# Performance work log

Measured on AMD Instinct MI355X. Metric: run time of the kernel, lower is better.

Reference implementation:

```python
import jax, jax.numpy as jnp
import numpy as np

N = 16384       # num nodes
E = 65536       # num edges (before self loops)
IN_DIM = 1536
HID = 1024
HEADS = 8
HD = HID // HEADS  # 128
NEG_SLOPE = 0.2
EPS = 1e-5


def _xavier(key, shape):
    fan_in, fan_out = shape[0], shape[-1]
    s = jnp.sqrt(6.0 / (fan_in + fan_out)).astype(jnp.float32)
    return jax.random.uniform(key, shape, jnp.float32, -s, s)


def setup_inputs() -> dict:
    key = jax.random.key(0)
    ks = jax.random.split(key, 32)
    inp = {
        "x": jax.random.normal(ks[0], (N, IN_DIM), jnp.float32),
        "edge_index": jax.random.randint(ks[1], (2, E), 0, N, dtype=jnp.int32),
        # input projection + norm1
        "W_in": _xavier(ks[2], (IN_DIM, HID)), "b_in": jnp.zeros((HID,), jnp.float32),
        "ln1_g": jnp.ones((HID,), jnp.float32), "ln1_b": jnp.zeros((HID,), jnp.float32),
        # GATv2 layer 1
        "g1_Wl": _xavier(ks[3], (HID, HID)), "g1_bl": jnp.zeros((HID,), jnp.float32),
        "g1_Wr": _xavier(ks[4], (HID, HID)), "g1_br": jnp.zeros((HID,), jnp.float32),
        "g1_att": _xavier(ks[5], (HEADS, HD)), "g1_bo": jnp.zeros((HID,), jnp.float32),
        "ln2_g": jnp.ones((HID,), jnp.float32), "ln2_b": jnp.zeros((HID,), jnp.float32),
        # GATv2 layer 2
        "g2_Wl": _xavier(ks[6], (HID, HID)), "g2_bl": jnp.zeros((HID,), jnp.float32),
        "g2_Wr": _xavier(ks[7], (HID, HID)), "g2_br": jnp.zeros((HID,), jnp.float32),
        "g2_att": _xavier(ks[8], (HEADS, HD)), "g2_bo": jnp.zeros((HID,), jnp.float32),
        "ln3_g": jnp.ones((HID,), jnp.float32), "ln3_b": jnp.zeros((HID,), jnp.float32),
        # scorer MLP 1024 -> 512 -> 128 -> 1
        "Ws1": _xavier(ks[9], (HID, 512)), "bs1": jnp.zeros((512,), jnp.float32),
        "Ws2": _xavier(ks[10], (512, 128)), "bs2": jnp.zeros((128,), jnp.float32),
        "Ws3": _xavier(ks[11], (128, 1)), "bs3": jnp.zeros((1,), jnp.float32),
    }
    return inp


def layer_norm(x, g, b):
    mu = jnp.mean(x, axis=-1, keepdims=True)
    var = jnp.var(x, axis=-1, keepdims=True)
    return (x - mu) * jax.lax.rsqrt(var + EPS) * g + b


def gatv2(h, src, dst, Wl, bl, Wr, br, att, bo):
    # GATv2Conv: x_j = lin_l(h)[src], x_i = lin_r(h)[dst]
    xl = (h @ Wl + bl).reshape(N, HEADS, HD)
    xr = (h @ Wr + br).reshape(N, HEADS, HD)
    e = jax.nn.leaky_relu(xl[src] + xr[dst], NEG_SLOPE)      # [E', H, C]
    logit = jnp.einsum('ehc,hc->eh', e, att)                  # [E', H]
    m = jax.ops.segment_max(logit, dst, num_segments=N)       # segment softmax over dst
    a = jnp.exp(logit - m[dst])
    denom = jax.ops.segment_sum(a, dst, num_segments=N)
    alpha = a / denom[dst]
    out = jax.ops.segment_sum(alpha[:, :, None] * xl[src], dst, num_segments=N)
    return out.reshape(N, HID) + bo


def reference(x, edge_index, W_in, b_in, ln1_g, ln1_b,
              g1_Wl, g1_bl, g1_Wr, g1_br, g1_att, g1_bo, ln2_g, ln2_b,
              g2_Wl, g2_bl, g2_Wr, g2_br, g2_att, g2_bo, ln3_g, ln3_b,
              Ws1, bs1, Ws2, bs2, Ws3, bs3):
    # PyG GATv2Conv adds self-loops by default
    loop = jnp.arange(N, dtype=edge_index.dtype)
    src = jnp.concatenate([edge_index[0], loop])
    dst = jnp.concatenate([edge_index[1], loop])

    h = jax.nn.gelu(layer_norm(x @ W_in + b_in, ln1_g, ln1_b), approximate=False)
    h1 = gatv2(h, src, dst, g1_Wl, g1_bl, g1_Wr, g1_br, g1_att, g1_bo)
    h = h + jax.nn.gelu(layer_norm(h1, ln2_g, ln2_b), approximate=False)
    h2 = gatv2(h, src, dst, g2_Wl, g2_bl, g2_Wr, g2_br, g2_att, g2_bo)
    h = h + jax.nn.gelu(layer_norm(h2, ln3_g, ln3_b), approximate=False)

    s = jax.nn.silu(h @ Ws1 + bs1)
    s = jax.nn.silu(s @ Ws2 + bs2)
    scores = (s @ Ws3 + bs3).squeeze(-1)   # [N]
    return scores, h
```

## Files before the change

kernel.cpp:

```cpp
#include <hip/hip_runtime.h>
#include <hip/hip_bf16.h>
#include <math.h>

#define N_NODES 16384
#define E_EDGES 65536
#define ET (E_EDGES + N_NODES)
#define IN_DIM 1536
#define HID 1024
#define XSTR 2048

typedef __attribute__((ext_vector_type(8))) short bf16x8;
typedef __attribute__((ext_vector_type(4))) float f32x4;

__device__ __forceinline__ unsigned short f2b(float f) {
  unsigned int u = __float_as_uint(f);
  u = (u + 0x7FFFu + ((u >> 16) & 1u)) >> 16;
  return (unsigned short)u;
}

__device__ __forceinline__ float b2f(unsigned short u) {
  return __uint_as_float((unsigned int)u << 16);
}

__device__ __forceinline__ void gload_lds16(const void* g, void* l) {
  __builtin_amdgcn_global_load_lds((const __attribute__((address_space(1))) void*)g,
                                   (__attribute__((address_space(3))) void*)l, 16, 0, 0);
}

__device__ __forceinline__ float gelu_exact(float y) {
  return 0.5f * y * (1.0f + erff(y * 0.70710678118654752f));
}

__global__ void conv_bf16_kernel(const float* __restrict__ in, unsigned short* __restrict__ out, int n4) {
  int i = blockIdx.x * 256 + threadIdx.x;
  if (i < n4) {
    float4 v = ((const float4*)in)[i];
    ushort4 o;
    o.x = f2b(v.x); o.y = f2b(v.y); o.z = f2b(v.z); o.w = f2b(v.w);
    ((ushort4*)out)[i] = o;
  }
}

__global__ void transpose_conv_kernel(const float* __restrict__ in, unsigned short* __restrict__ out,
                                      int K, int N) {
  __shared__ float tile[32][33];
  int bx = blockIdx.x * 32;
  int by = blockIdx.y * 32;
  int tx = threadIdx.x, ty = threadIdx.y;
  #pragma unroll
  for (int i = 0; i < 32; i += 8)
    tile[ty + i][tx] = in[(size_t)(by + ty + i) * N + bx + tx];
  __syncthreads();
  #pragma unroll
  for (int i = 0; i < 32; i += 8)
    out[(size_t)(bx + ty + i) * K + by + tx] = f2b(tile[tx][ty + i]);
}

__global__ void concat2_kernel(const float* __restrict__ a, const float* __restrict__ b,
                               float* __restrict__ o, int n) {
  int i = blockIdx.x * 256 + threadIdx.x;
  if (i < n) o[i] = a[i];
  else if (i < 2 * n) o[i] = b[i - n];
}

template <int ACT, int WB>
__global__ __launch_bounds__(512)
void gemm_bf16_kernel(const unsigned short* __restrict__ A, const unsigned short* __restrict__ Bt,
                      const float* __restrict__ bias, float* __restrict__ C,
                      unsigned short* __restrict__ Cb, int M, int N, int K, int nx) {
  __shared__ unsigned short As[256 * 64];
  __shared__ unsigned short Bs[128 * 64];
  const int t = threadIdx.x;
  const int l = t & 63;
  const int w = t >> 6;
  const int wr = w >> 1, wc = w & 1;

  const int nwg = gridDim.x;
  const int bid = blockIdx.x;
  int tile = bid;
  if ((nwg & 7) == 0) {
    const int cpx = nwg >> 3;
    tile = (bid & 7) * cpx + (bid >> 3);
  }
  const int bm = (tile / nx) * 256;
  const int bn = (tile % nx) * 128;

  f32x4 acc[4][4];
  #pragma unroll
  for (int m = 0; m < 4; m++)
    #pragma unroll
    for (int n = 0; n < 4; n++) acc[m][n] = (f32x4){0.f, 0.f, 0.f, 0.f};

  const int srow = t >> 3;
  const int scolbsw = ((t & 7) * 16) ^ ((srow & 7) << 4);
  const unsigned short* Ag = A + (size_t)(bm + srow) * K + (scolbsw >> 1);
  const unsigned short* Bg = Bt + (size_t)(bn + srow) * K + (scolbsw >> 1);

  const int ar = wr * 64 + (l & 15);
  const int br = wc * 64 + (l & 15);
  const int kk2 = (l >> 4) * 16;
  const int swA = (ar & 7) << 4;
  const int swB = (br & 7) << 4;
  const char* Asb = (const char*)As;
  const char* Bsb = (const char*)Bs;

  for (int k0 = 0; k0 < K; k0 += 64) {
    #pragma unroll
    for (int i = 0; i < 4; i++)
      gload_lds16(Ag + (size_t)i * 64 * K + k0, (char*)As + t * 16 + i * 8192);
    #pragma unroll
    for (int i = 0; i < 2; i++)
      gload_lds16(Bg + (size_t)i * 64 * K + k0, (char*)Bs + t * 16 + i * 8192);
    __syncthreads();
    bf16x8 af[4], bfr[4];
    #pragma unroll
    for (int kh = 0; kh < 2; kh++) {
      const int kb = kk2 + kh * 64;
      #pragma unroll
      for (int m = 0; m < 4; m++)
        af[m] = *(const bf16x8*)(Asb + (ar + m * 16) * 128 + (kb ^ swA));
      #pragma unroll
      for (int n = 0; n < 4; n++)
        bfr[n] = *(const bf16x8*)(Bsb + (br + n * 16) * 128 + (kb ^ swB));
      #pragma unroll
      for (int m = 0; m < 4; m++)
        #pragma unroll
        for (int n = 0; n < 4; n++)
          acc[m][n] = __builtin_amdgcn_mfma_f32_16x16x32_bf16(af[m], bfr[n], acc[m][n], 0, 0, 0);
    }
    __syncthreads();
  }

  const int crow0 = bm + wr * 64 + (l >> 4) * 4;
  const int ccol0 = bn + wc * 64 + (l & 15);
  #pragma unroll
  for (int m = 0; m < 4; m++) {
    #pragma unroll
    for (int n = 0; n < 4; n++) {
      int col = ccol0 + n * 16;
      float bv = bias[col];
      #pragma unroll
      for (int v = 0; v < 4; v++) {
        int row = crow0 + m * 16 + v;
        float x = acc[m][n][v] + bv;
        if (ACT == 1) x = x / (1.0f + expf(-x));
        if (WB != 2) C[(size_t)row * N + col] = x;
        if (WB != 0) Cb[(size_t)row * N + col] = f2b(x);
      }
    }
  }
}

__global__ __launch_bounds__(256)
void ln_gelu_kernel(const float* __restrict__ c, const float* __restrict__ g,
                    const float* __restrict__ b, float* __restrict__ h,
                    unsigned short* __restrict__ hb) {
  int row = blockIdx.x;
  int t = threadIdx.x;
  const float* cr = c + (size_t)row * HID;
  float v[4];
  float s = 0.f, q = 0.f;
  #pragma unroll
  for (int j = 0; j < 4; j++) {
    v[j] = cr[t + 256 * j];
    s += v[j];
    q += v[j] * v[j];
  }
  #pragma unroll
  for (int off = 32; off; off >>= 1) {
    s += __shfl_xor(s, off);
    q += __shfl_xor(q, off);
  }
  __shared__ float rs[4], rq[4];
  int wv = t >> 6, l = t & 63;
  if (l == 0) { rs[wv] = s; rq[wv] = q; }
  __syncthreads();
  s = rs[0] + rs[1] + rs[2] + rs[3];
  q = rq[0] + rq[1] + rq[2] + rq[3];
  float mu = s * (1.0f / HID);
  float var = q * (1.0f / HID) - mu * mu;
  float rstd = rsqrtf(var + 1e-5f);
  float* hr = h + (size_t)row * HID;
  unsigned short* hbr = hb + (size_t)row * HID;
  #pragma unroll
  for (int j = 0; j < 4; j++) {
    int ci = t + 256 * j;
    float y = (v[j] - mu) * rstd * g[ci] + b[ci];
    float z = gelu_exact(y);
    hr[ci] = z;
    hbr[ci] = f2b(z);
  }
}

__global__ void build_edges_kernel(const int* __restrict__ ei, int* __restrict__ srcA,
                                   int* __restrict__ dstA, int* __restrict__ deg) {
  int i = blockIdx.x * 256 + threadIdx.x;
  if (i >= ET) return;
  int s, d;
  if (i < E_EDGES) { s = ei[i]; d = ei[E_EDGES + i]; }
  else             { s = i - E_EDGES; d = s; }
  srcA[i] = s;
  dstA[i] = d;
  atomicAdd(&deg[d], 1);
}

__global__ __launch_bounds__(1024)
void scan16k_kernel(const int* __restrict__ deg, int* __restrict__ rowstart) {
  __shared__ int s[1024];
  int t = threadIdx.x;
  int local[16];
  int sum = 0;
  #pragma unroll
  for (int i = 0; i < 16; i++) { local[i] = deg[t * 16 + i]; sum += local[i]; }
  s[t] = sum;
  __syncthreads();
  for (int off = 1; off < 1024; off <<= 1) {
    int v = (t >= off) ? s[t - off] : 0;
    __syncthreads();
    s[t] += v;
    __syncthreads();
  }
  int run = s[t] - sum;
  #pragma unroll
  for (int i = 0; i < 16; i++) { rowstart[t * 16 + i] = run; run += local[i]; }
  if (t == 1023) rowstart[16384] = run;
}

__global__ void scatter_edges_kernel(const int* __restrict__ srcA, const int* __restrict__ dstA,
                                     const int* __restrict__ rowstart, int* __restrict__ cursor,
                                     int* __restrict__ src_csr) {
  int i = blockIdx.x * 256 + threadIdx.x;
  if (i >= ET) return;
  int d = dstA[i];
  int pos = atomicAdd(&cursor[d], 1);
  src_csr[rowstart[d] + pos] = srcA[i];
}

__global__ __launch_bounds__(256)
void gat_fused_kernel(const unsigned short* __restrict__ xe, const float* __restrict__ att,
                      const int* __restrict__ src_csr, const int* __restrict__ rowstart,
                      const float* __restrict__ bo, const float* __restrict__ lng,
                      const float* __restrict__ lnb, float* __restrict__ h,
                      unsigned short* __restrict__ hb) {
  const int nid = blockIdx.x;
  const int beg = rowstart[nid], end = rowstart[nid + 1];
  const int d = end - beg;
  const int t = threadIdx.x;
  const int l = t & 63;
  const int wid = t >> 6;
  const int hh = t >> 5;
  const int c0 = t * 4;

  __shared__ unsigned short xl_s[8][1024];
  __shared__ float lg_s[8][8];

  float xrf[16], attf[16];
  {
    const unsigned short* xrd = xe + (size_t)nid * XSTR + 1024 + l * 16;
    bf16x8 r0 = *(const bf16x8*)xrd;
    bf16x8 r1 = *(const bf16x8*)(xrd + 8);
    #pragma unroll
    for (int j = 0; j < 8; j++) {
      xrf[j] = b2f((unsigned short)r0[j]);
      xrf[j + 8] = b2f((unsigned short)r1[j]);
    }
    const float4 A0 = *(const float4*)(att + l * 16);
    const float4 A1 = *(const float4*)(att + l * 16 + 4);
    const float4 A2 = *(const float4*)(att + l * 16 + 8);
    const float4 A3 = *(const float4*)(att + l * 16 + 12);
    attf[0] = A0.x; attf[1] = A0.y; attf[2] = A0.z; attf[3] = A0.w;
    attf[4] = A1.x; attf[5] = A1.y; attf[6] = A1.z; attf[7] = A1.w;
    attf[8] = A2.x; attf[9] = A2.y; attf[10] = A2.z; attf[11] = A2.w;
    attf[12] = A3.x; attf[13] = A3.y; attf[14] = A3.z; attf[15] = A3.w;
  }

  float m = -1e30f, den = 0.f;
  float a0 = 0.f, a1 = 0.f, a2 = 0.f, a3 = 0.f;

  for (int chunk = 0; chunk < d; chunk += 8) {
    int cn = min(8, d - chunk);
    for (int e = wid; e < cn; e += 4) {
      int s = src_csr[beg + chunk + e];
      const unsigned short* xls = xe + (size_t)s * XSTR + l * 16;
      bf16x8 x0 = *(const bf16x8*)xls;
      bf16x8 x1 = *(const bf16x8*)(xls + 8);
      *(bf16x8*)&xl_s[e][l * 16] = x0;
      *(bf16x8*)&xl_s[e][l * 16 + 8] = x1;
      float p = 0.f;
      #pragma unroll
      for (int j = 0; j < 8; j++) {
        float u = b2f((unsigned short)x0[j]) + xrf[j];
        float v = b2f((unsigned short)x1[j]) + xrf[j + 8];
        u = u > 0.f ? u : 0.2f * u;
        v = v > 0.f ? v : 0.2f * v;
        p += u * attf[j] + v * attf[j + 8];
      }
      p += __shfl_xor(p, 1);
      p += __shfl_xor(p, 2);
      p += __shfl_xor(p, 4);
      if ((l & 7) == 0) lg_s[e][l >> 3] = p;
    }
    __syncthreads();
    float cm = -1e30f;
    for (int i = 0; i < cn; i++) cm = fmaxf(cm, lg_s[i][hh]);
    float nm = fmaxf(m, cm);
    float sc = expf(m - nm);
    a0 *= sc; a1 *= sc; a2 *= sc; a3 *= sc; den *= sc;
    for (int i = 0; i < cn; i++) {
      float wgt = expf(lg_s[i][hh] - nm);
      den += wgt;
      ushort4 v = *(const ushort4*)&xl_s[i][c0];
      a0 += wgt * b2f(v.x);
      a1 += wgt * b2f(v.y);
      a2 += wgt * b2f(v.z);
      a3 += wgt * b2f(v.w);
    }
    m = nm;
    __syncthreads();
  }

  float inv = 1.0f / den;
  const float4 bv = *(const float4*)(bo + c0);
  float v0 = a0 * inv + bv.x, v1 = a1 * inv + bv.y;
  float v2 = a2 * inv + bv.z, v3 = a3 * inv + bv.w;
  float s = v0 + v1 + v2 + v3;
  float q = v0 * v0 + v1 * v1 + v2 * v2 + v3 * v3;
  #pragma unroll
  for (int off = 32; off; off >>= 1) {
    s += __shfl_xor(s, off);
    q += __shfl_xor(q, off);
  }
  __shared__ float rs[4], rq[4];
  int wv = t >> 6, ll = t & 63;
  if (ll == 0) { rs[wv] = s; rq[wv] = q; }
  __syncthreads();
  s = rs[0] + rs[1] + rs[2] + rs[3];
  q = rq[0] + rq[1] + rq[2] + rq[3];
  float mu = s * (1.0f / HID);
  float var = q * (1.0f / HID) - mu * mu;
  float rstd = rsqrtf(var + 1e-5f);
  const float4 gv = *(const float4*)(lng + c0);
  const float4 bbv = *(const float4*)(lnb + c0);
  float* hr = h + (size_t)nid * HID;
  float4 hold = *(const float4*)(hr + c0);
  float o0 = hold.x + gelu_exact((v0 - mu) * rstd * gv.x + bbv.x);
  float o1 = hold.y + gelu_exact((v1 - mu) * rstd * gv.y + bbv.y);
  float o2 = hold.z + gelu_exact((v2 - mu) * rstd * gv.z + bbv.z);
  float o3 = hold.w + gelu_exact((v3 - mu) * rstd * gv.w + bbv.w);
  *(float4*)(hr + c0) = (float4){o0, o1, o2, o3};
  ushort4 ob;
  ob.x = f2b(o0); ob.y = f2b(o1); ob.z = f2b(o2); ob.w = f2b(o3);
  *(ushort4*)(hb + (size_t)nid * HID + c0) = ob;
}

__global__ __launch_bounds__(256)
void score_kernel(const float* __restrict__ s2, const float* __restrict__ Ws3,
                  const float* __restrict__ bs3, float* __restrict__ out) {
  int nid = blockIdx.x * 4 + (threadIdx.x >> 6);
  int l = threadIdx.x & 63;
  const float* r = s2 + (size_t)nid * 128;
  float a = r[l] * Ws3[l] + r[l + 64] * Ws3[l + 64];
  #pragma unroll
  for (int off = 32; off; off >>= 1) a += __shfl_xor(a, off);
  if (l == 0) out[nid] = a + bs3[0];
}

extern "C" void kernel_launch(void* const* d_in, const int* in_sizes, int n_in,
                              void* d_out, int out_size, void* d_ws, size_t ws_size,
                              hipStream_t stream) {
  const float* x    = (const float*)d_in[0];
  const int*   ei   = (const int*)  d_in[1];
  const float* W_in = (const float*)d_in[2];
  const float* b_in = (const float*)d_in[3];
  const float* ln1g = (const float*)d_in[4];
  const float* ln1b = (const float*)d_in[5];
  const float* g1Wl = (const float*)d_in[6];
  const float* g1bl = (const float*)d_in[7];
  const float* g1Wr = (const float*)d_in[8];
  const float* g1br = (const float*)d_in[9];
  const float* g1att= (const float*)d_in[10];
  const float* g1bo = (const float*)d_in[11];
  const float* ln2g = (const float*)d_in[12];
  const float* ln2b = (const float*)d_in[13];
  const float* g2Wl = (const float*)d_in[14];
  const float* g2bl = (const float*)d_in[15];
  const float* g2Wr = (const float*)d_in[16];
  const float* g2br = (const float*)d_in[17];
  const float* g2att= (const float*)d_in[18];
  const float* g2bo = (const float*)d_in[19];
  const float* ln3g = (const float*)d_in[20];
  const float* ln3b = (const float*)d_in[21];
  const float* Ws1  = (const float*)d_in[22];
  const float* bs1  = (const float*)d_in[23];
  const float* Ws2  = (const float*)d_in[24];
  const float* bs2  = (const float*)d_in[25];
  const float* Ws3  = (const float*)d_in[26];
  const float* bs3  = (const float*)d_in[27];

  float* scores = (float*)d_out;
  float* h      = (float*)d_out + N_NODES;

  char* wsp = (char*)d_ws;
  size_t off = 0;
  auto alloc = [&](size_t bytes) -> char* {
    char* p = wsp + off;
    off += (bytes + 255) & ~(size_t)255;
    return p;
  };
  unsigned short* xb    = (unsigned short*)alloc((size_t)N_NODES * IN_DIM * 2);
  unsigned short* WinT  = (unsigned short*)alloc((size_t)HID * IN_DIM * 2);
  unsigned short* g1WT  = (unsigned short*)alloc((size_t)XSTR * HID * 2);
  unsigned short* g2WT  = (unsigned short*)alloc((size_t)XSTR * HID * 2);
  unsigned short* Ws1T  = (unsigned short*)alloc((size_t)512 * HID * 2);
  unsigned short* Ws2T  = (unsigned short*)alloc((size_t)128 * 512 * 2);
  unsigned short* hb    = (unsigned short*)alloc((size_t)N_NODES * HID * 2);
  unsigned short* s1b   = (unsigned short*)alloc((size_t)N_NODES * 512 * 2);
  unsigned short* xe    = (unsigned short*)alloc((size_t)N_NODES * XSTR * 2);
  float* bcat1  = (float*)alloc((size_t)XSTR * 4);
  float* bcat2  = (float*)alloc((size_t)XSTR * 4);
  float* C      = (float*)alloc((size_t)N_NODES * HID * 4);
  int* srcA     = (int*)alloc((size_t)ET * 4);
  int* dstA     = (int*)alloc((size_t)ET * 4);
  int* deg      = (int*)alloc(65536);
  int* cursor   = (int*)alloc(65536);
  int* rowstart = (int*)alloc(65544);
  int* src_csr  = (int*)alloc((size_t)ET * 4);

  conv_bf16_kernel<<<(N_NODES * IN_DIM / 4 + 255) / 256, 256, 0, stream>>>(x, xb, N_NODES * IN_DIM / 4);
  dim3 tb(32, 8);
  transpose_conv_kernel<<<dim3(HID / 32, IN_DIM / 32), tb, 0, stream>>>(W_in, WinT, IN_DIM, HID);
  transpose_conv_kernel<<<dim3(HID / 32, HID / 32), tb, 0, stream>>>(g1Wl, g1WT, HID, HID);
  transpose_conv_kernel<<<dim3(HID / 32, HID / 32), tb, 0, stream>>>(g1Wr, g1WT + (size_t)HID * HID, HID, HID);
  transpose_conv_kernel<<<dim3(HID / 32, HID / 32), tb, 0, stream>>>(g2Wl, g2WT, HID, HID);
  transpose_conv_kernel<<<dim3(HID / 32, HID / 32), tb, 0, stream>>>(g2Wr, g2WT + (size_t)HID * HID, HID, HID);
  transpose_conv_kernel<<<dim3(512 / 32, HID / 32), tb, 0, stream>>>(Ws1, Ws1T, HID, 512);
  transpose_conv_kernel<<<dim3(128 / 32, 512 / 32), tb, 0, stream>>>(Ws2, Ws2T, 512, 128);
  concat2_kernel<<<XSTR / 256, 256, 0, stream>>>(g1bl, g1br, bcat1, HID);
  concat2_kernel<<<XSTR / 256, 256, 0, stream>>>(g2bl, g2br, bcat2, HID);

  hipMemsetAsync(deg, 0, 131072, stream);
  build_edges_kernel<<<ET / 256, 256, 0, stream>>>(ei, srcA, dstA, deg);
  scan16k_kernel<<<1, 1024, 0, stream>>>(deg, rowstart);
  scatter_edges_kernel<<<ET / 256, 256, 0, stream>>>(srcA, dstA, rowstart, cursor, src_csr);

  gemm_bf16_kernel<0, 0><<<(N_NODES / 256) * (HID / 128), 512, 0, stream>>>(
      xb, WinT, b_in, C, nullptr, N_NODES, HID, IN_DIM, HID / 128);
  ln_gelu_kernel<<<N_NODES, 256, 0, stream>>>(C, ln1g, ln1b, h, hb);

  gemm_bf16_kernel<0, 2><<<(N_NODES / 256) * (XSTR / 128), 512, 0, stream>>>(
      hb, g1WT, bcat1, nullptr, xe, N_NODES, XSTR, HID, XSTR / 128);
  gat_fused_kernel<<<N_NODES, 256, 0, stream>>>(xe, g1att, src_csr, rowstart, g1bo,
                                                ln2g, ln2b, h, hb);

  gemm_bf16_kernel<0, 2><<<(N_NODES / 256) * (XSTR / 128), 512, 0, stream>>>(
      hb, g2WT, bcat2, nullptr, xe, N_NODES, XSTR, HID, XSTR / 128);
  gat_fused_kernel<<<N_NODES, 256, 0, stream>>>(xe, g2att, src_csr, rowstart, g2bo,
                                                ln3g, ln3b, h, hb);

  gemm_bf16_kernel<1, 2><<<(N_NODES / 256) * (512 / 128), 512, 0, stream>>>(
      hb, Ws1T, bs1, nullptr, s1b, N_NODES, 512, HID, 512 / 128);
  gemm_bf16_kernel<1, 0><<<(N_NODES / 256) * 1, 512, 0, stream>>>(
      s1b, Ws2T, bs2, C, nullptr, N_NODES, 128, 512, 1);
  score_kernel<<<N_NODES / 4, 256, 0, stream>>>(C, Ws3, bs3, scores);
}
```

Measured before the change: 529.9 us.

## Process one node per wavefront in GAT aggregation with register online softmax

Restructures the fused GATv2 aggregation so each 64-lane wavefront handles one destination node. Each lane keeps 16 channels in registers and runs an online softmax per edge, so the shared-memory staging and block barriers are gone. The next edge's source row is prefetched while the current one is processed, and the layer norm reduction stays within the wave. The trade is serial per-edge latency within a wave and higher register use in exchange for removing barriers and LDS traffic.

```diff
diff --git a/kernel.cpp b/kernel.cpp
--- a/kernel.cpp
+++ b/kernel.cpp
@@ -242,21 +242,14 @@
                       const float* __restrict__ bo, const float* __restrict__ lng,
                       const float* __restrict__ lnb, float* __restrict__ h,
                       unsigned short* __restrict__ hb) {
-  const int nid = blockIdx.x;
+  const int l = threadIdx.x & 63;
+  const int nid = blockIdx.x * 4 + (threadIdx.x >> 6);
   const int beg = rowstart[nid], end = rowstart[nid + 1];
-  const int d = end - beg;
-  const int t = threadIdx.x;
-  const int l = t & 63;
-  const int wid = t >> 6;
-  const int hh = t >> 5;
-  const int c0 = t * 4;
-
-  __shared__ unsigned short xl_s[8][1024];
-  __shared__ float lg_s[8][8];
+  const int cb = l * 16;
 
   float xrf[16], attf[16];
   {
-    const unsigned short* xrd = xe + (size_t)nid * XSTR + 1024 + l * 16;
+    const unsigned short* xrd = xe + (size_t)nid * XSTR + 1024 + cb;
     bf16x8 r0 = *(const bf16x8*)xrd;
     bf16x8 r1 = *(const bf16x8*)(xrd + 8);
     #pragma unroll
@@ -264,93 +257,95 @@
       xrf[j] = b2f((unsigned short)r0[j]);
       xrf[j + 8] = b2f((unsigned short)r1[j]);
     }
-    const float4 A0 = *(const float4*)(att + l * 16);
-    const float4 A1 = *(const float4*)(att + l * 16 + 4);
-    const float4 A2 = *(const float4*)(att + l * 16 + 8);
-    const float4 A3 = *(const float4*)(att + l * 16 + 12);
-    attf[0] = A0.x; attf[1] = A0.y; attf[2] = A0.z; attf[3] = A0.w;
-    attf[4] = A1.x; attf[5] = A1.y; attf[6] = A1.z; attf[7] = A1.w;
-    attf[8] = A2.x; attf[9] = A2.y; attf[10] = A2.z; attf[11] = A2.w;
-    attf[12] = A3.x; attf[13] = A3.y; attf[14] = A3.z; attf[15] = A3.w;
+    #pragma unroll
+    for (int j = 0; j < 4; j++) {
+      float4 a = *(const float4*)(att + cb + j * 4);
+      attf[j * 4] = a.x; attf[j * 4 + 1] = a.y;
+      attf[j * 4 + 2] = a.z; attf[j * 4 + 3] = a.w;
+    }
   }
 
   float m = -1e30f, den = 0.f;
-  float a0 = 0.f, a1 = 0.f, a2 = 0.f, a3 = 0.f;
-
-  for (int chunk = 0; chunk < d; chunk += 8) {
-    int cn = min(8, d - chunk);
-    for (int e = wid; e < cn; e += 4) {
-      int s = src_csr[beg + chunk + e];
-      const unsigned short* xls = xe + (size_t)s * XSTR + l * 16;
-      bf16x8 x0 = *(const bf16x8*)xls;
-      bf16x8 x1 = *(const bf16x8*)(xls + 8);
-      *(bf16x8*)&xl_s[e][l * 16] = x0;
-      *(bf16x8*)&xl_s[e][l * 16 + 8] = x1;
-      float p = 0.f;
-      #pragma unroll
-      for (int j = 0; j < 8; j++) {
-        float u = b2f((unsigned short)x0[j]) + xrf[j];
-        float v = b2f((unsigned short)x1[j]) + xrf[j + 8];
-        u = u > 0.f ? u : 0.2f * u;
-        v = v > 0.f ? v : 0.2f * v;
-        p += u * attf[j] + v * attf[j + 8];
-      }
-      p += __shfl_xor(p, 1);
-      p += __shfl_xor(p, 2);
-      p += __shfl_xor(p, 4);
-      if ((l & 7) == 0) lg_s[e][l >> 3] = p;
-    }
-    __syncthreads();
-    float cm = -1e30f;
-    for (int i = 0; i < cn; i++) cm = fmaxf(cm, lg_s[i][hh]);
-    float nm = fmaxf(m, cm);
+  float acc[16];
+  #pragma unroll
+  for (int j = 0; j < 16; j++) acc[j] = 0.f;
+
+  bf16x8 x0, x1;
+  if (beg < end) {
+    const unsigned short* xls = xe + (size_t)src_csr[beg] * XSTR + cb;
+    x0 = *(const bf16x8*)xls;
+    x1 = *(const bf16x8*)(xls + 8);
+  }
+  for (int e = beg; e < end; ++e) {
+    bf16x8 c0 = x0, c1 = x1;
+    if (e + 1 < end) {
+      const unsigned short* xls = xe + (size_t)src_csr[e + 1] * XSTR + cb;
+      x0 = *(const bf16x8*)xls;
+      x1 = *(const bf16x8*)(xls + 8);
+    }
+    float xf[16];
+    #pragma unroll
+    for (int j = 0; j < 8; j++) {
+      xf[j] = b2f((unsigned short)c0[j]);
+      xf[j + 8] = b2f((unsigned short)c1[j]);
+    }
+    float p = 0.f;
+    #pragma unroll
+    for (int j = 0; j < 16; j++) {
+      float u = xf[j] + xrf[j];
+      u = u > 0.f ? u : 0.2f * u;
+      p += u * attf[j];
+    }
+    p += __shfl_xor(p, 1);
+    p += __shfl_xor(p, 2);
+    p += __shfl_xor(p, 4);
+    float nm = fmaxf(m, p);
     float sc = expf(m - nm);
-    a0 *= sc; a1 *= sc; a2 *= sc; a3 *= sc; den *= sc;
-    for (int i = 0; i < cn; i++) {
-      float wgt = expf(lg_s[i][hh] - nm);
-      den += wgt;
-      ushort4 v = *(const ushort4*)&xl_s[i][c0];
-      a0 += wgt * b2f(v.x);
-      a1 += wgt * b2f(v.y);
-      a2 += wgt * b2f(v.z);
-      a3 += wgt * b2f(v.w);
-    }
+    float wgt = expf(p - nm);
+    den = den * sc + wgt;
+    #pragma unroll
+    for (int j = 0; j < 16; j++) acc[j] = acc[j] * sc + wgt * xf[j];
     m = nm;
-    __syncthreads();
   }
 
   float inv = 1.0f / den;
-  const float4 bv = *(const float4*)(bo + c0);
-  float v0 = a0 * inv + bv.x, v1 = a1 * inv + bv.y;
-  float v2 = a2 * inv + bv.z, v3 = a3 * inv + bv.w;
-  float s = v0 + v1 + v2 + v3;
-  float q = v0 * v0 + v1 * v1 + v2 * v2 + v3 * v3;
+  float v[16];
+  #pragma unroll
+  for (int j = 0; j < 4; j++) {
+    float4 b = *(const float4*)(bo + cb + j * 4);
+    v[j * 4] = acc[j * 4] * inv + b.x;
+    v[j * 4 + 1] = acc[j * 4 + 1] * inv + b.y;
+    v[j * 4 + 2] = acc[j * 4 + 2] * inv + b.z;
+    v[j * 4 + 3] = acc[j * 4 + 3] * inv + b.w;
+  }
+  float s = 0.f, q = 0.f;
+  #pragma unroll
+  for (int j = 0; j < 16; j++) { s += v[j]; q += v[j] * v[j]; }
   #pragma unroll
   for (int off = 32; off; off >>= 1) {
     s += __shfl_xor(s, off);
     q += __shfl_xor(q, off);
   }
-  __shared__ float rs[4], rq[4];
-  int wv = t >> 6, ll = t & 63;
-  if (ll == 0) { rs[wv] = s; rq[wv] = q; }
-  __syncthreads();
-  s = rs[0] + rs[1] + rs[2] + rs[3];
-  q = rq[0] + rq[1] + rq[2] + rq[3];
   float mu = s * (1.0f / HID);
   float var = q * (1.0f / HID) - mu * mu;
   float rstd = rsqrtf(var + 1e-5f);
-  const float4 gv = *(const float4*)(lng + c0);
-  const float4 bbv = *(const float4*)(lnb + c0);
-  float* hr = h + (size_t)nid * HID;
-  float4 hold = *(const float4*)(hr + c0);
-  float o0 = hold.x + gelu_exact((v0 - mu) * rstd * gv.x + bbv.x);
-  float o1 = hold.y + gelu_exact((v1 - mu) * rstd * gv.y + bbv.y);
-  float o2 = hold.z + gelu_exact((v2 - mu) * rstd * gv.z + bbv.z);
-  float o3 = hold.w + gelu_exact((v3 - mu) * rstd * gv.w + bbv.w);
-  *(float4*)(hr + c0) = (float4){o0, o1, o2, o3};
-  ushort4 ob;
-  ob.x = f2b(o0); ob.y = f2b(o1); ob.z = f2b(o2); ob.w = f2b(o3);
-  *(ushort4*)(hb + (size_t)nid * HID + c0) = ob;
+
+  float* hr = h + (size_t)nid * HID + cb;
+  unsigned short* hbr = hb + (size_t)nid * HID + cb;
+  #pragma unroll
+  for (int j = 0; j < 4; j++) {
+    float4 gv = *(const float4*)(lng + cb + j * 4);
+    float4 bb = *(const float4*)(lnb + cb + j * 4);
+    float4 hold = *(const float4*)(hr + j * 4);
+    float o0 = hold.x + gelu_exact((v[j * 4] - mu) * rstd * gv.x + bb.x);
+    float o1 = hold.y + gelu_exact((v[j * 4 + 1] - mu) * rstd * gv.y + bb.y);
+    float o2 = hold.z + gelu_exact((v[j * 4 + 2] - mu) * rstd * gv.z + bb.z);
+    float o3 = hold.w + gelu_exact((v[j * 4 + 3] - mu) * rstd * gv.w + bb.w);
+    *(float4*)(hr + j * 4) = (float4){o0, o1, o2, o3};
+    ushort4 ob;
+    ob.x = f2b(o0); ob.y = f2b(o1); ob.z = f2b(o2); ob.w = f2b(o3);
+    *(ushort4*)(hbr + j * 4) = ob;
+  }
 }
 
 __global__ __launch_bounds__(256)
@@ -449,13 +444,13 @@
 
   gemm_bf16_kernel<0, 2><<<(N_NODES / 256) * (XSTR / 128), 512, 0, stream>>>(
       hb, g1WT, bcat1, nullptr, xe, N_NODES, XSTR, HID, XSTR / 128);
-  gat_fused_kernel<<<N_NODES, 256, 0, stream>>>(xe, g1att, src_csr, rowstart, g1bo,
-                                                ln2g, ln2b, h, hb);
+  gat_fused_kernel<<<N_NODES / 4, 256, 0, stream>>>(xe, g1att, src_csr, rowstart, g1bo,
+                                                    ln2g, ln2b, h, hb);
 
   gemm_bf16_kernel<0, 2><<<(N_NODES / 256) * (XSTR / 128), 512, 0, stream>>>(
       hb, g2WT, bcat2, nullptr, xe, N_NODES, XSTR, HID, XSTR / 128);
-  gat_fused_kernel<<<N_NODES, 256, 0, stream>>>(xe, g2att, src_csr, rowstart, g2bo,
-                                                ln3g, ln3b, h, hb);
+  gat_fused_kernel<<<N_NODES / 4, 256, 0, stream>>>(xe, g2att, src_csr, rowstart, g2bo,
+                                                    ln3g, ln3b, h, hb);
 
   gemm_bf16_kernel<1, 2><<<(N_NODES / 256) * (512 / 128), 512, 0, stream>>>(
       hb, Ws1T, bs1, nullptr, s1b, N_NODES, 512, HID, 512 / 128);
```

Result: faster. 499.4 us (-5.8%).
